# Performance work log

Measured on AMD Instinct MI355X. Metric: run time of the kernel, lower is better.

## Reference

```python
import jax, jax.numpy as jnp
import numpy as np

N, IN_DIM, HID, OUT = 100000, 256, 256, 128
E = 500000


def setup_inputs() -> dict:
    key = jax.random.key(0)
    ks = jax.random.split(key, 12)
    s_in = 1.0 / np.sqrt(IN_DIM)
    s_h = 1.0 / np.sqrt(HID)
    s_c = 1.0 / np.sqrt(2 * OUT)
    return {
        "x": jax.random.normal(ks[0], (N, IN_DIM), dtype=jnp.float32),
        "pos_u": jax.random.randint(ks[1], (E,), 0, N),
        "pos_v": jax.random.randint(ks[2], (E,), 0, N),
        "neg_u": jax.random.randint(ks[3], (E,), 0, N),
        "neg_v": jax.random.randint(ks[4], (E,), 0, N),
        "Wn1": jax.random.normal(ks[5], (IN_DIM, HID), dtype=jnp.float32) * s_in,
        "bn1": jnp.zeros((HID,), dtype=jnp.float32),
        "Wn2": jax.random.normal(ks[6], (HID, OUT), dtype=jnp.float32) * s_h,
        "bn2": jnp.zeros((OUT,), dtype=jnp.float32),
        "Ws1": jax.random.normal(ks[7], (2 * OUT, HID), dtype=jnp.float32) * s_c,
        "bs1": jnp.zeros((HID,), dtype=jnp.float32),
        "Ws2": jax.random.normal(ks[8], (HID, 1), dtype=jnp.float32) * s_h,
        "bs2": jnp.zeros((1,), dtype=jnp.float32),
    }


def _pair_logits(H, u, v, Ws1, bs1, Ws2, bs2):
    hu = H[u]  # [E, OUT] gather
    hv = H[v]
    feats = jnp.concatenate([jnp.abs(hu - hv), hu * hv], axis=-1)  # [E, 2*OUT]
    h = jax.nn.relu(feats @ Ws1 + bs1)
    return (h @ Ws2 + bs2)[..., 0]  # [E]


def reference(x, pos_u, pos_v, neg_u, neg_v,
              Wn1, bn1, Wn2, bn2, Ws1, bs1, Ws2, bs2):
    # node encoder MLP (dropout = identity in eval)
    H = jax.nn.relu(x @ Wn1 + bn1) @ Wn2 + bn2  # [N, OUT]
    pos_logit = _pair_logits(H, pos_u, pos_v, Ws1, bs1, Ws2, bs2)
    neg_logit = _pair_logits(H, neg_u, neg_v, Ws1, bs1, Ws2, bs2)
    return (pos_logit, neg_logit, H)
```

## Files before the change

kernel.cpp:

```cpp
#include <hip/hip_runtime.h>

typedef unsigned short u16;
typedef __bf16 bf16x8 __attribute__((ext_vector_type(8)));
typedef float f32x4 __attribute__((ext_vector_type(4)));
typedef unsigned int u32x4 __attribute__((ext_vector_type(4)));

#define MFMA16(a, b, c) __builtin_amdgcn_mfma_f32_16x16x32_bf16((a), (b), (c), 0, 0, 0)

#define NNODE 100000
#define EDGES 500000
#define NPAIR 1000000

__device__ __forceinline__ u16 bf16bits(float f) {
  __bf16 h = (__bf16)f;
  return __builtin_bit_cast(unsigned short, h);
}

__global__ void prep_weights(const float* __restrict__ Wn1,
                             const float* __restrict__ Wn2,
                             const float* __restrict__ Ws1,
                             u16* __restrict__ ws) {
  int gid = blockIdx.x * 256 + threadIdx.x;
  const float* src;
  int ldn;
  u16* dst;
  int e;
  if (gid < 65536) {
    src = Wn1; ldn = 256; dst = ws; e = gid;
  } else if (gid < 98304) {
    src = Wn2; ldn = 128; dst = ws + 65536; e = gid - 65536;
  } else {
    src = Ws1; ldn = 256; dst = ws + 98304; e = gid - 98304;
  }
  int j = e & 7;
  int lane = (e >> 3) & 63;
  int s = (e >> 9) & 7;
  int nt = e >> 12;
  int n = (nt << 4) | (lane & 15);
  int k = (s << 5) | (((lane >> 4) & 3) << 3) | j;
  dst[e] = bf16bits(src[k * ldn + n]);
}

__launch_bounds__(256, 2)
__global__ void node_kernel(const float* __restrict__ x,
                            const u16* __restrict__ WnT1,
                            const u16* __restrict__ WnT2,
                            const float* __restrict__ bn1,
                            const float* __restrict__ bn2,
                            float* __restrict__ Hout,
                            u16* __restrict__ Hb) {
  __shared__ __align__(16) u16 buf[32768];
  const int tid = threadIdx.x;
  const int w = tid >> 6, l = tid & 63;
  const int lg = l >> 4, ll = l & 15;
  const int rowbase = blockIdx.x * 128 + w * 32;

  bf16x8 af[2][8];
#pragma unroll
  for (int m = 0; m < 2; m++) {
    int r = rowbase + m * 16 + ll;
    if (r > NNODE - 1) r = NNODE - 1;
    const float* xp = x + (long)r * 256 + lg * 8;
#pragma unroll
    for (int c = 0; c < 8; c++) {
      f32x4 a0 = *(const f32x4*)(xp + c * 32);
      f32x4 a1 = *(const f32x4*)(xp + c * 32 + 4);
      bf16x8 d;
#pragma unroll
      for (int j = 0; j < 4; j++) {
        d[j] = (__bf16)a0[j];
        d[j + 4] = (__bf16)a1[j];
      }
      af[m][c] = d;
    }
  }

  f32x4 acc[2][16];
#pragma unroll
  for (int nh = 0; nh < 2; nh++) {
    if (nh) __syncthreads();
    {
      const u32x4* src = (const u32x4*)(WnT1 + nh * 32768);
      u32x4* dstv = (u32x4*)buf;
#pragma unroll
      for (int i = 0; i < 16; i++) dstv[tid + i * 256] = src[tid + i * 256];
    }
    __syncthreads();
#pragma unroll
    for (int nt = 0; nt < 8; nt++) {
      int n = nh * 128 + nt * 16 + ll;
      float bv = bn1[n];
      f32x4 a0 = {bv, bv, bv, bv}, a1 = a0;
      const u16* bp = buf + nt * 4096 + l * 8;
#pragma unroll
      for (int s = 0; s < 8; s++) {
        bf16x8 bw = *(const bf16x8*)(bp + s * 512);
        a0 = MFMA16(af[0][s], bw, a0);
        a1 = MFMA16(af[1][s], bw, a1);
      }
      acc[0][nh * 8 + nt] = a0;
      acc[1][nh * 8 + nt] = a1;
    }
  }
  __syncthreads();

  const int hbase = w * 8192;
#pragma unroll
  for (int m = 0; m < 2; m++) {
#pragma unroll
    for (int q = 0; q < 16; q++) {
      int s2 = q >> 1;
      int k3 = ((q & 1) << 1) | (ll >> 3);
      int j = ll & 7;
      f32x4 a = acc[m][q];
#pragma unroll
      for (int t = 0; t < 4; t++) {
        int lane2 = k3 * 16 + lg * 4 + t;
        buf[hbase + ((m * 8 + s2) * 64 + lane2) * 8 + j] = bf16bits(fmaxf(a[t], 0.f));
      }
    }
  }

#pragma unroll
  for (int m = 0; m < 2; m++) {
#pragma unroll
    for (int s = 0; s < 8; s++) {
      af[m][s] = *(const bf16x8*)(buf + hbase + ((m * 8 + s) * 64 + l) * 8);
    }
  }

#pragma unroll
  for (int nt = 0; nt < 8; nt++) {
    int n = nt * 16 + ll;
    float bv = bn2[n];
    f32x4 a0 = {bv, bv, bv, bv}, a1 = a0;
    const u16* bp = WnT2 + nt * 4096 + l * 8;
#pragma unroll
    for (int s = 0; s < 8; s++) {
      bf16x8 bw = *(const bf16x8*)(bp + s * 512);
      a0 = MFMA16(af[0][s], bw, a0);
      a1 = MFMA16(af[1][s], bw, a1);
    }
#pragma unroll
    for (int t = 0; t < 4; t++) {
      int r0 = rowbase + lg * 4 + t;
      if (r0 < NNODE) {
        Hout[(long)r0 * 128 + n] = a0[t];
        if (Hb) Hb[(long)r0 * 128 + n] = bf16bits(a0[t]);
      }
      int r1 = rowbase + 16 + lg * 4 + t;
      if (r1 < NNODE) {
        Hout[(long)r1 * 128 + n] = a1[t];
        if (Hb) Hb[(long)r1 * 128 + n] = bf16bits(a1[t]);
      }
    }
  }
}

template <bool BF16H>
__launch_bounds__(512, 1)
__global__ void pair_kernel9(const void* __restrict__ Hsrc,
                             const int* __restrict__ pos_u,
                             const int* __restrict__ pos_v,
                             const int* __restrict__ neg_u,
                             const int* __restrict__ neg_v,
                             const u16* __restrict__ WsT,
                             const float* __restrict__ bs1,
                             const float* __restrict__ Ws2,
                             const float* __restrict__ bs2,
                             float* __restrict__ out) {
  __shared__ __align__(16) u16 buf[32768];
  const int tid = threadIdx.x;
  const int w = tid >> 6, l = tid & 63;
  const int lg = l >> 4, ll = l & 15;
  const float b2 = bs2[0];

  {
    const u32x4* src = (const u32x4*)WsT;
    u32x4* dstv = (u32x4*)buf;
#pragma unroll
    for (int i = 0; i < 8; i++) dstv[tid + i * 512] = src[tid + i * 512];
  }
  __syncthreads();

  int res = 0;
  const int nchunks = (NPAIR + 255) / 256;
  for (int chunk = blockIdx.x; chunk < nchunks; chunk += gridDim.x) {
    const int base = chunk * 256 + w * 32;

    bf16x8 af[2][8];
#pragma unroll
    for (int m = 0; m < 2; m++) {
      int p = base + m * 16 + ll;
      int pc = (p < NPAIR) ? p : (NPAIR - 1);
      bool pos = pc < EDGES;
      int idx = pos ? pc : pc - EDGES;
      const int* ul = pos ? pos_u : neg_u;
      const int* vl = pos ? pos_v : neg_v;
      int u = ul[idx];
      int v = vl[idx];
      if constexpr (BF16H) {
        const u16* hu = (const u16*)Hsrc + (long)u * 128 + lg * 8;
        const u16* hv = (const u16*)Hsrc + (long)v * 128 + lg * 8;
#pragma unroll
        for (int c = 0; c < 4; c++) {
          bf16x8 a = *(const bf16x8*)(hu + c * 32);
          bf16x8 b = *(const bf16x8*)(hv + c * 32);
          bf16x8 d = a - b;
          u32x4 du = __builtin_bit_cast(u32x4, d) & 0x7FFF7FFFu;
          af[m][c] = __builtin_bit_cast(bf16x8, du);
          af[m][c + 4] = a * b;
        }
      } else {
        const float* hu = (const float*)Hsrc + (long)u * 128 + lg * 8;
        const float* hv = (const float*)Hsrc + (long)v * 128 + lg * 8;
#pragma unroll
        for (int c = 0; c < 4; c++) {
          f32x4 a0 = *(const f32x4*)(hu + c * 32);
          f32x4 a1 = *(const f32x4*)(hu + c * 32 + 4);
          f32x4 b0 = *(const f32x4*)(hv + c * 32);
          f32x4 b1 = *(const f32x4*)(hv + c * 32 + 4);
          bf16x8 d, pr;
#pragma unroll
          for (int j = 0; j < 4; j++) {
            d[j] = (__bf16)__builtin_fabsf(a0[j] - b0[j]);
            d[j + 4] = (__bf16)__builtin_fabsf(a1[j] - b1[j]);
            pr[j] = (__bf16)(a0[j] * b0[j]);
            pr[j + 4] = (__bf16)(a1[j] * b1[j]);
          }
          af[m][c] = d;
          af[m][c + 4] = pr;
        }
      }
      __builtin_amdgcn_sched_barrier(0);
    }

    float lp[2][4] = {};

#pragma unroll
    for (int nt = 0; nt < 8; nt++) {
      int n = res * 128 + nt * 16 + ll;
      float bv = bs1[n];
      f32x4 acc0 = {bv, bv, bv, bv}, acc1 = acc0;
      const u16* bp = buf + nt * 4096 + l * 8;
#pragma unroll
      for (int s = 0; s < 8; s++) {
        bf16x8 bw = *(const bf16x8*)(bp + s * 512);
        acc0 = MFMA16(af[0][s], bw, acc0);
        acc1 = MFMA16(af[1][s], bw, acc1);
      }
      float w2 = Ws2[n];
#pragma unroll
      for (int t = 0; t < 4; t++) {
        lp[0][t] += fmaxf(acc0[t], 0.f) * w2;
        lp[1][t] += fmaxf(acc1[t], 0.f) * w2;
      }
    }

    __syncthreads();
    {
      const u32x4* src = (const u32x4*)(WsT + (res ^ 1) * 32768);
      u32x4* dstv = (u32x4*)buf;
#pragma unroll
      for (int i = 0; i < 8; i++) dstv[tid + i * 512] = src[tid + i * 512];
    }
    __syncthreads();

#pragma unroll
    for (int nt = 0; nt < 8; nt++) {
      int n = (res ^ 1) * 128 + nt * 16 + ll;
      float bv = bs1[n];
      f32x4 acc0 = {bv, bv, bv, bv}, acc1 = acc0;
      const u16* bp = buf + nt * 4096 + l * 8;
#pragma unroll
      for (int s = 0; s < 8; s++) {
        bf16x8 bw = *(const bf16x8*)(bp + s * 512);
        acc0 = MFMA16(af[0][s], bw, acc0);
        acc1 = MFMA16(af[1][s], bw, acc1);
      }
      float w2 = Ws2[n];
#pragma unroll
      for (int t = 0; t < 4; t++) {
        lp[0][t] += fmaxf(acc0[t], 0.f) * w2;
        lp[1][t] += fmaxf(acc1[t], 0.f) * w2;
      }
    }
    res ^= 1;

#pragma unroll
    for (int m = 0; m < 2; m++) {
#pragma unroll
      for (int t = 0; t < 4; t++) {
        float v = lp[m][t];
        v += __shfl_xor(v, 1, 16);
        v += __shfl_xor(v, 2, 16);
        v += __shfl_xor(v, 4, 16);
        v += __shfl_xor(v, 8, 16);
        int p = base + m * 16 + lg * 4 + t;
        if (ll == 0 && p < NPAIR) out[p] = v + b2;
      }
    }
  }
}

extern "C" void kernel_launch(void* const* d_in, const int* in_sizes, int n_in,
                              void* d_out, int out_size, void* d_ws, size_t ws_size,
                              hipStream_t stream) {
  (void)in_sizes; (void)n_in; (void)out_size;
  const float* x = (const float*)d_in[0];
  const int* pos_u = (const int*)d_in[1];
  const int* pos_v = (const int*)d_in[2];
  const int* neg_u = (const int*)d_in[3];
  const int* neg_v = (const int*)d_in[4];
  const float* Wn1 = (const float*)d_in[5];
  const float* bn1 = (const float*)d_in[6];
  const float* Wn2 = (const float*)d_in[7];
  const float* bn2 = (const float*)d_in[8];
  const float* Ws1 = (const float*)d_in[9];
  const float* bs1 = (const float*)d_in[10];
  const float* Ws2 = (const float*)d_in[11];
  const float* bs2 = (const float*)d_in[12];
  float* out = (float*)d_out;
  u16* wsp = (u16*)d_ws;

  float* Hout = out + NPAIR;
  const size_t need = 327680 + (size_t)NNODE * 128 * 2;
  const bool bf16h = ws_size >= need;
  u16* Hb = bf16h ? (wsp + 163840) : nullptr;

  prep_weights<<<640, 256, 0, stream>>>(Wn1, Wn2, Ws1, wsp);
  node_kernel<<<(NNODE + 127) / 128, 256, 0, stream>>>(x, wsp, wsp + 65536, bn1, bn2,
                                                       Hout, Hb);
  if (bf16h) {
    pair_kernel9<true><<<512, 512, 0, stream>>>(Hb, pos_u, pos_v, neg_u, neg_v,
                                                wsp + 98304, bs1, Ws2, bs2, out);
  } else {
    pair_kernel9<false><<<512, 512, 0, stream>>>(Hout, pos_u, pos_v, neg_u, neg_v,
                                                 wsp + 98304, bs1, Ws2, bs2, out);
  }
}
```

Before: 279.7 us.

## Shrink pair kernel blocks to 256 threads with quarter-sized LDS weight slices

Halves the pair-scoring block to 256 threads and processes 128 pairs per chunk, streaming the first-layer score weights through LDS in four 64-column slices instead of two halves. The smaller LDS footprint and launch bounds allow several blocks per CU, raising occupancy to hide gather latency. The cost is more frequent weight reloads into LDS, more barriers per pair, and a tighter register budget that may cause spills.

```diff
diff --git a/kernel.cpp b/kernel.cpp
--- a/kernel.cpp
+++ b/kernel.cpp
@@ -158,18 +158,18 @@
 }
 
 template <bool BF16H>
-__launch_bounds__(512, 1)
-__global__ void pair_kernel9(const void* __restrict__ Hsrc,
-                             const int* __restrict__ pos_u,
-                             const int* __restrict__ pos_v,
-                             const int* __restrict__ neg_u,
-                             const int* __restrict__ neg_v,
-                             const u16* __restrict__ WsT,
-                             const float* __restrict__ bs1,
-                             const float* __restrict__ Ws2,
-                             const float* __restrict__ bs2,
-                             float* __restrict__ out) {
-  __shared__ __align__(16) u16 buf[32768];
+__launch_bounds__(256, 4)
+__global__ void pair_kernel10(const void* __restrict__ Hsrc,
+                              const int* __restrict__ pos_u,
+                              const int* __restrict__ pos_v,
+                              const int* __restrict__ neg_u,
+                              const int* __restrict__ neg_v,
+                              const u16* __restrict__ WsT,
+                              const float* __restrict__ bs1,
+                              const float* __restrict__ Ws2,
+                              const float* __restrict__ bs2,
+                              float* __restrict__ out) {
+  __shared__ __align__(16) u16 buf[16384];
   const int tid = threadIdx.x;
   const int w = tid >> 6, l = tid & 63;
   const int lg = l >> 4, ll = l & 15;
@@ -179,14 +179,14 @@
     const u32x4* src = (const u32x4*)WsT;
     u32x4* dstv = (u32x4*)buf;
 #pragma unroll
-    for (int i = 0; i < 8; i++) dstv[tid + i * 512] = src[tid + i * 512];
+    for (int i = 0; i < 8; i++) dstv[tid + i * 256] = src[tid + i * 256];
   }
   __syncthreads();
 
   int res = 0;
-  const int nchunks = (NPAIR + 255) / 256;
+  const int nchunks = (NPAIR + 127) / 128;
   for (int chunk = blockIdx.x; chunk < nchunks; chunk += gridDim.x) {
-    const int base = chunk * 256 + w * 32;
+    const int base = chunk * 128 + w * 32;
 
     bf16x8 af[2][8];
 #pragma unroll
@@ -236,56 +236,38 @@
     }
 
     float lp[2][4] = {};
-
-#pragma unroll
-    for (int nt = 0; nt < 8; nt++) {
-      int n = res * 128 + nt * 16 + ll;
-      float bv = bs1[n];
-      f32x4 acc0 = {bv, bv, bv, bv}, acc1 = acc0;
-      const u16* bp = buf + nt * 4096 + l * 8;
-#pragma unroll
-      for (int s = 0; s < 8; s++) {
-        bf16x8 bw = *(const bf16x8*)(bp + s * 512);
-        acc0 = MFMA16(af[0][s], bw, acc0);
-        acc1 = MFMA16(af[1][s], bw, acc1);
-      }
-      float w2 = Ws2[n];
-#pragma unroll
-      for (int t = 0; t < 4; t++) {
-        lp[0][t] += fmaxf(acc0[t], 0.f) * w2;
-        lp[1][t] += fmaxf(acc1[t], 0.f) * w2;
-      }
-    }
-
-    __syncthreads();
-    {
-      const u32x4* src = (const u32x4*)(WsT + (res ^ 1) * 32768);
-      u32x4* dstv = (u32x4*)buf;
-#pragma unroll
-      for (int i = 0; i < 8; i++) dstv[tid + i * 512] = src[tid + i * 512];
-    }
-    __syncthreads();
-
-#pragma unroll
-    for (int nt = 0; nt < 8; nt++) {
-      int n = (res ^ 1) * 128 + nt * 16 + ll;
-      float bv = bs1[n];
-      f32x4 acc0 = {bv, bv, bv, bv}, acc1 = acc0;
-      const u16* bp = buf + nt * 4096 + l * 8;
-#pragma unroll
-      for (int s = 0; s < 8; s++) {
-        bf16x8 bw = *(const bf16x8*)(bp + s * 512);
-        acc0 = MFMA16(af[0][s], bw, acc0);
-        acc1 = MFMA16(af[1][s], bw, acc1);
-      }
-      float w2 = Ws2[n];
-#pragma unroll
-      for (int t = 0; t < 4; t++) {
-        lp[0][t] += fmaxf(acc0[t], 0.f) * w2;
-        lp[1][t] += fmaxf(acc1[t], 0.f) * w2;
-      }
-    }
-    res ^= 1;
+#pragma unroll
+    for (int q = 0; q < 4; q++) {
+      const int cur = (res + q) & 3;
+      if (q) {
+        __syncthreads();
+        const u32x4* src = (const u32x4*)(WsT + cur * 16384);
+        u32x4* dstv = (u32x4*)buf;
+#pragma unroll
+        for (int i = 0; i < 8; i++) dstv[tid + i * 256] = src[tid + i * 256];
+        __syncthreads();
+      }
+#pragma unroll
+      for (int nt = 0; nt < 4; nt++) {
+        int n = cur * 64 + nt * 16 + ll;
+        float bv = bs1[n];
+        f32x4 acc0 = {bv, bv, bv, bv}, acc1 = acc0;
+        const u16* bp = buf + nt * 4096 + l * 8;
+#pragma unroll
+        for (int s = 0; s < 8; s++) {
+          bf16x8 bw = *(const bf16x8*)(bp + s * 512);
+          acc0 = MFMA16(af[0][s], bw, acc0);
+          acc1 = MFMA16(af[1][s], bw, acc1);
+        }
+        float w2 = Ws2[n];
+#pragma unroll
+        for (int t = 0; t < 4; t++) {
+          lp[0][t] += fmaxf(acc0[t], 0.f) * w2;
+          lp[1][t] += fmaxf(acc1[t], 0.f) * w2;
+        }
+      }
+    }
+    res = (res + 3) & 3;
 
 #pragma unroll
     for (int m = 0; m < 2; m++) {
@@ -332,10 +314,10 @@
   node_kernel<<<(NNODE + 127) / 128, 256, 0, stream>>>(x, wsp, wsp + 65536, bn1, bn2,
                                                        Hout, Hb);
   if (bf16h) {
-    pair_kernel9<true><<<512, 512, 0, stream>>>(Hb, pos_u, pos_v, neg_u, neg_v,
-                                                wsp + 98304, bs1, Ws2, bs2, out);
+    pair_kernel10<true><<<1024, 256, 0, stream>>>(Hb, pos_u, pos_v, neg_u, neg_v,
+                                                  wsp + 98304, bs1, Ws2, bs2, out);
   } else {
-    pair_kernel9<false><<<512, 512, 0, stream>>>(Hout, pos_u, pos_v, neg_u, neg_v,
-                                                 wsp + 98304, bs1, Ws2, bs2, out);
-  }
-}
+    pair_kernel10<false><<<1024, 256, 0, stream>>>(Hout, pos_u, pos_v, neg_u, neg_v,
+                                                   wsp + 98304, bs1, Ws2, bs2, out);
+  }
+}
```

New measurement: 450.1 us. 1.61x slower.
